# Performance work log

Hardware: AMD Instinct MI355X
Metric: run time of the kernel (lower is better)

Reference implementation:

```python
import jax, jax.numpy as jnp
import numpy as np
import math

N_HEAD = 8
N_EMBD = 1024
HEAD_DIM = N_EMBD // N_HEAD // 2  # 64
LAYER_IDX = 4
LAMBDA_INIT = 0.8 - 0.6 * math.exp(-0.3 * LAYER_IDX)
RMS_EPS = float(jnp.finfo(jnp.float32).eps)  # torch RMSNorm eps=None default
LN_EPS = 1e-5


def rmsnorm(x):
    return x * jax.lax.rsqrt(jnp.mean(x * x, axis=-1, keepdims=True) + RMS_EPS)


def layernorm(x):
    mu = jnp.mean(x, axis=-1, keepdims=True)
    var = jnp.mean(jnp.square(x - mu), axis=-1, keepdims=True)
    return (x - mu) * jax.lax.rsqrt(var + LN_EPS)


def rope_tables(T, dim, dtype):
    inv_freq = 1.0 / (10000.0 ** (np.arange(0, dim, 2, dtype=np.float32) / dim))
    t = np.arange(T, dtype=np.float32)
    freqs = np.outer(t, inv_freq)  # [T, dim/2]
    return jnp.asarray(np.cos(freqs), dtype), jnp.asarray(np.sin(freqs), dtype)


def apply_rotary(x, cos, sin):
    # x: [B, T, H, D]; cos/sin: [T, D/2]
    d = x.shape[-1] // 2
    x1, x2 = x[..., :d], x[..., d:]
    c = cos[None, :, None, :]
    s = sin[None, :, None, :]
    return jnp.concatenate([x1 * c + x2 * s, -x1 * s + x2 * c], axis=-1)


def setup_inputs() -> dict:
    key = jax.random.key(0)
    ks = jax.random.split(key, 9)
    B, T, C = 4, 2048, N_EMBD
    scale = 1.0 / math.sqrt(C)
    return {
        "x": jax.random.normal(ks[0], (B, T, C), jnp.float32),
        "Wq": jax.random.normal(ks[1], (C, C), jnp.float32) * scale,
        "Wk": jax.random.normal(ks[2], (C, C), jnp.float32) * scale,
        "Wv": jax.random.normal(ks[3], (C, C), jnp.float32) * scale,
        "Wproj": jax.random.normal(ks[4], (C, C), jnp.float32) * scale,
        "lq1": jax.random.normal(ks[5], (HEAD_DIM,), jnp.float32) * 0.1,
        "lk1": jax.random.normal(ks[6], (HEAD_DIM,), jnp.float32) * 0.1,
        "lq2": jax.random.normal(ks[7], (HEAD_DIM,), jnp.float32) * 0.1,
        "lk2": jax.random.normal(ks[8], (HEAD_DIM,), jnp.float32) * 0.1,
    }


def reference(x, Wq, Wk, Wv, Wproj, lq1, lk1, lq2, lk2):
    B, T, C = x.shape
    H, hd = N_HEAD, HEAD_DIM
    q = (x @ Wq.T).reshape(B, T, 2 * H, hd)
    k = (x @ Wk.T).reshape(B, T, 2 * H, hd)
    v = (x @ Wv.T).reshape(B, T, H, 2 * hd)

    cos, sin = rope_tables(T, hd, x.dtype)
    q = apply_rotary(rmsnorm(q), cos, sin)
    k = apply_rotary(rmsnorm(k), cos, sin)

    q = jnp.transpose(q, (0, 2, 1, 3)) * (1.0 / math.sqrt(hd))  # [B, 2H, T, hd]
    k = jnp.transpose(k, (0, 2, 1, 3))
    v = jnp.transpose(v, (0, 2, 1, 3))  # [B, H, T, 2hd]

    scores = jnp.einsum('bhqd,bhkd->bhqk', q, k)  # [B, 2H, T, T]
    causal = jnp.tril(jnp.ones((T, T), bool))
    scores = jnp.where(causal[None, None], scores, -jnp.inf)
    attn = jax.nn.softmax(scores.astype(jnp.float32), axis=-1).astype(scores.dtype)

    attn = attn.reshape(B, H, 2, T, T)
    lam1 = jnp.exp(jnp.sum(lq1 * lk1))
    lam2 = jnp.exp(jnp.sum(lq2 * lk2))
    lam = lam1 - lam2 + LAMBDA_INIT
    attn = attn[:, :, 0] - lam * attn[:, :, 1]  # [B, H, T, T]

    out = jnp.einsum('bhqk,bhkd->bhqd', attn, v)  # [B, H, T, 2hd]
    out = layernorm(out) * (1.0 - LAMBDA_INIT)
    out = jnp.transpose(out, (0, 2, 1, 3)).reshape(B, T, C)
    return out @ Wproj.T
```

## Files before the change

kernel.cpp:

```cpp
#include <hip/hip_runtime.h>
#include <hip/hip_bf16.h>
#include <math.h>


typedef __bf16 bf16_t;
typedef __bf16 bf16x8 __attribute__((ext_vector_type(8)));
typedef __bf16 bf16x4 __attribute__((ext_vector_type(4)));
typedef float  f32x4  __attribute__((ext_vector_type(4)));

#define T_SEQ 2048
#define C_EMB 1024
static constexpr float LAMBDA_INIT = 0.6192834728526787f;
static constexpr float ONE_MINUS_LI = 0.3807165271473213f;
static constexpr float RMS_EPS = 1.1920928955078125e-07f;
static constexpr float LN_EPS = 1e-5f;
static constexpr float M_FIX = 9.0f;

__device__ __forceinline__ f32x4 mfma16(bf16x8 a, bf16x8 b, f32x4 c) {
  return __builtin_amdgcn_mfma_f32_16x16x32_bf16(a, b, c, 0, 0, 0);
}
__device__ __forceinline__ float declamp(float v, float lim) {
  return fminf(fmaxf(v, -lim), lim);
}
__device__ __forceinline__ void ldsload16(const bf16_t* g, bf16_t* l) {
  __builtin_amdgcn_global_load_lds(
      (const __attribute__((address_space(1))) void*)g,
      (__attribute__((address_space(3))) void*)l, 16, 0, 0);
}


__global__ __launch_bounds__(256) void cvt_all(
    const float* __restrict__ x,  const float* __restrict__ Wq,
    const float* __restrict__ Wk, const float* __restrict__ Wv,
    const float* __restrict__ Wp,
    bf16_t* __restrict__ xb,  bf16_t* __restrict__ wqb, bf16_t* __restrict__ wkb,
    bf16_t* __restrict__ wvb, bf16_t* __restrict__ wpb)
{
  size_t i4 = ((size_t)blockIdx.x * 256 + threadIdx.x) * 4;
  const float* s; bf16_t* d; size_t off;
  if      (i4 <  8388608) { s = x;  d = xb;  off = i4; }
  else if (i4 <  9437184) { s = Wq; d = wqb; off = i4 - 8388608; }
  else if (i4 < 10485760) { s = Wk; d = wkb; off = i4 - 9437184; }
  else if (i4 < 11534336) { s = Wv; d = wvb; off = i4 - 10485760; }
  else                    { s = Wp; d = wpb; off = i4 - 11534336; }
  f32x4 v = *(const f32x4*)(s + off);
  bf16x4 bv;
#pragma unroll
  for (int j = 0; j < 4; ++j) bv[j] = (bf16_t)v[j];
  *(bf16x4*)(d + off) = bv;
}

__device__ __forceinline__ void gemm_core(
    const bf16_t* __restrict__ A, const bf16_t* __restrict__ W,
    bf16_t* As, bf16_t* Bs, f32x4 acc[4][4], int m0, int n0)
{
  const int tid = threadIdx.x;
  const int lane = tid & 63, w = tid >> 6;
  const int wm = w >> 1, wn = w & 1;
  const int l15 = lane & 15, quad = lane >> 4;
  for (int k0 = 0; k0 < C_EMB; k0 += 32) {
#pragma unroll
    for (int i = 0; i < 2; ++i) {
      int c = tid + i * 256;
      int r = c >> 2, c8 = (c & 3) * 8;
      *(bf16x8*)&As[r * 40 + c8] = *(const bf16x8*)&A[(size_t)(m0 + r) * C_EMB + k0 + c8];
      *(bf16x8*)&Bs[r * 40 + c8] = *(const bf16x8*)&W[(size_t)(n0 + r) * C_EMB + k0 + c8];
    }
    __syncthreads();
    bf16x8 af[4], bfr[4];
#pragma unroll
    for (int i = 0; i < 4; ++i)
      af[i] = *(const bf16x8*)&As[(wm * 64 + i * 16 + l15) * 40 + quad * 8];
#pragma unroll
    for (int j = 0; j < 4; ++j)
      bfr[j] = *(const bf16x8*)&Bs[(wn * 64 + j * 16 + l15) * 40 + quad * 8];
#pragma unroll
    for (int i = 0; i < 4; ++i)
#pragma unroll
      for (int j = 0; j < 4; ++j) acc[i][j] = mfma16(af[i], bfr[j], acc[i][j]);
    __syncthreads();
  }
}

__global__ __launch_bounds__(256) void gemm_qkv(
    const bf16_t* __restrict__ A,
    const bf16_t* __restrict__ Wqb, const bf16_t* __restrict__ Wkb, const bf16_t* __restrict__ Wvb,
    bf16_t* __restrict__ qo, bf16_t* __restrict__ ko, bf16_t* __restrict__ vt)
{
  const int z = blockIdx.z;
  const bf16_t* W = (z == 0) ? Wqb : ((z == 1) ? Wkb : Wvb);
  const int n0 = blockIdx.x * 128, m0 = blockIdx.y * 128;
  __shared__ bf16_t As[128 * 40];
  __shared__ bf16_t Bs[128 * 40];
  const int lane = threadIdx.x & 63, w = threadIdx.x >> 6;
  const int wm = w >> 1, wn = w & 1;
  const int l15 = lane & 15, quad = lane >> 4;
  const f32x4 fz = {0.f, 0.f, 0.f, 0.f};
  f32x4 acc[4][4];
#pragma unroll
  for (int i = 0; i < 4; ++i)
#pragma unroll
    for (int j = 0; j < 4; ++j) acc[i][j] = fz;
  gemm_core(A, W, As, Bs, acc, m0, n0);

  if (z < 2) {
    bf16_t* C = z ? ko : qo;
#pragma unroll
    for (int i = 0; i < 4; ++i)
#pragma unroll
      for (int j = 0; j < 4; ++j)
#pragma unroll
        for (int r = 0; r < 4; ++r) {
          int row = m0 + wm * 64 + i * 16 + quad * 4 + r;
          int col = n0 + wn * 64 + j * 16 + l15;
          C[(size_t)row * C_EMB + col] = (bf16_t)declamp(acc[i][j][r], 1e4f);
        }
  } else {
#pragma unroll
    for (int i = 0; i < 4; ++i)
#pragma unroll
      for (int j = 0; j < 4; ++j) {
        int row = m0 + wm * 64 + i * 16 + quad * 4;
        int col = n0 + wn * 64 + j * 16 + l15;
        bf16x4 pv;
#pragma unroll
        for (int r = 0; r < 4; ++r) pv[r] = (bf16_t)declamp(acc[i][j][r], 1e4f);
        size_t idx = (size_t)(row >> 11) * 2097152 + (size_t)col * 2048 + (row & 2047);
        *(bf16x4*)&vt[idx] = pv;
      }
  }
}

__global__ __launch_bounds__(256) void gemm_proj(
    const bf16_t* __restrict__ A, const bf16_t* __restrict__ Wpb, float* __restrict__ C)
{
  const int n0 = blockIdx.x * 128, m0 = blockIdx.y * 128;
  __shared__ bf16_t As[128 * 40];
  __shared__ bf16_t Bs[128 * 40];
  const int lane = threadIdx.x & 63, w = threadIdx.x >> 6;
  const int wm = w >> 1, wn = w & 1;
  const int l15 = lane & 15, quad = lane >> 4;
  const f32x4 fz = {0.f, 0.f, 0.f, 0.f};
  f32x4 acc[4][4];
#pragma unroll
  for (int i = 0; i < 4; ++i)
#pragma unroll
    for (int j = 0; j < 4; ++j) acc[i][j] = fz;
  gemm_core(A, Wpb, As, Bs, acc, m0, n0);
#pragma unroll
  for (int i = 0; i < 4; ++i)
#pragma unroll
    for (int j = 0; j < 4; ++j)
#pragma unroll
      for (int r = 0; r < 4; ++r) {
        int row = m0 + wm * 64 + i * 16 + quad * 4 + r;
        int col = n0 + wn * 64 + j * 16 + l15;
        C[(size_t)row * C_EMB + col] = declamp(acc[i][j][r], 1e4f);
      }
}

__global__ __launch_bounds__(256) void rope_rms2(bf16_t* __restrict__ q, bf16_t* __restrict__ k)
{
  bf16_t* arr = blockIdx.y ? k : q;
  const float scale = blockIdx.y ? 1.0f : 0.125f;
  const int tid = threadIdx.x;
  const int g = blockIdx.x * 16 + (tid >> 4);
  const int l16 = tid & 15;
  const int t = (g >> 4) & (T_SEQ - 1);
  bf16_t* p = arr + (size_t)g * 64 + l16 * 4;

  bf16x4 xv = *(const bf16x4*)p;
  float x[4];
#pragma unroll
  for (int j = 0; j < 4; ++j) x[j] = (float)xv[j];
  float ss = x[0]*x[0] + x[1]*x[1] + x[2]*x[2] + x[3]*x[3];
#pragma unroll
  for (int mm = 1; mm <= 8; mm <<= 1) ss += __shfl_xor(ss, mm);
  const float rn = rsqrtf(fmaxf(ss, 0.f) * (1.0f / 64.0f) + RMS_EPS);
  float nrm[4], prt[4];
#pragma unroll
  for (int j = 0; j < 4; ++j) nrm[j] = x[j] * rn;
#pragma unroll
  for (int j = 0; j < 4; ++j) prt[j] = __shfl_xor(nrm[j], 8);

  const int ib = (l16 & 7) * 4;
  const float sgn = (l16 < 8) ? 1.f : -1.f;
  bf16x4 ov;
#pragma unroll
  for (int j = 0; j < 4; ++j) {
    int i = ib + j;
    float invf = expf(-(float)i * 0.28782313662425575f);
    float ang = (float)t * invf;
    float c = cosf(ang), s = sinf(ang);
    ov[j] = (bf16_t)((nrm[j] * c + sgn * prt[j] * s) * scale);
  }
  *(bf16x4*)p = ov;
}

__device__ __forceinline__ void attn_step_fm(
    const bf16_t* __restrict__ ks, bf16_t* __restrict__ pw, const bf16_t* __restrict__ vts,
    const bf16x8* qf, float* rsum, f32x4* o,
    bool diag, int k0, int q0, int w, int l15, int quad)
{
  const int xs = l15 & 7;
  f32x4 sc[4];
#pragma unroll
  for (int nt = 0; nt < 4; ++nt) {
    f32x4 a = {0.f, 0.f, 0.f, 0.f};
#pragma unroll
    for (int s = 0; s < 2; ++s) {
      bf16x8 b = *(const bf16x8*)&ks[(nt * 16 + l15) * 64 + ((((s << 2) + quad) ^ xs) << 3)];
      a = mfma16(qf[s], b, a);
    }
#pragma unroll
    for (int r = 0; r < 4; ++r) a[r] = declamp(a[r], 30.f);
    sc[nt] = a;
  }
  if (diag) {
#pragma unroll
    for (int nt = 0; nt < 4; ++nt)
#pragma unroll
      for (int r = 0; r < 4; ++r) {
        int col = k0 + nt * 16 + l15;
        int row = q0 + w * 16 + quad * 4 + r;
        if (col > row) sc[nt][r] = -1e30f;
      }
  }
#pragma unroll
  for (int nt = 0; nt < 4; ++nt)
#pragma unroll
    for (int r = 0; r < 4; ++r) {
      float pv = __expf(sc[nt][r] - M_FIX);
      rsum[r] += pv;
      int row = quad * 4 + r;
      int col = nt * 16 + l15;
      pw[row * 64 + ((((col >> 3) ^ (row & 7)) << 3) | (col & 7))] = (bf16_t)pv;
    }
  __builtin_amdgcn_s_setprio(1);
#pragma unroll
  for (int s = 0; s < 2; ++s) {
    bf16x8 pa = *(const bf16x8*)&pw[l15 * 64 + ((((s << 2) + quad) ^ xs) << 3)];
#pragma unroll
    for (int nt2 = 0; nt2 < 8; ++nt2) {
      bf16x8 vb = *(const bf16x8*)&vts[(nt2 * 16 + l15) * 64 + ((((s << 2) + quad) ^ xs) << 3)];
      o[nt2] = mfma16(pa, vb, o[nt2]);
    }
  }
  __builtin_amdgcn_s_setprio(0);
}

__global__ __launch_bounds__(256) void diff_attn2(
    const bf16_t* __restrict__ qp, const bf16_t* __restrict__ kp, const bf16_t* __restrict__ vtp,
    const float* __restrict__ lq1, const float* __restrict__ lk1,
    const float* __restrict__ lq2, const float* __restrict__ lk2,
    bf16_t* __restrict__ outp)
{
  const int bh = blockIdx.x;
  const int bx = 31 - blockIdx.y;
  const int b = bh >> 3, h = bh & 7;
  const int q0 = bx * 64;
  const int tid = threadIdx.x;
  const int lane = tid & 63, w = tid >> 6;
  const int l15 = lane & 15, quad = lane >> 4;
  const size_t bT = (size_t)b * T_SEQ;
  const bf16_t* vth = vtp + (size_t)b * 2097152 + (size_t)(h * 128) * 2048;

  __shared__ bf16_t k1s[2][64 * 64];
  __shared__ bf16_t k2s[2][64 * 64];
  __shared__ bf16_t vts[2][128 * 64];
  __shared__ bf16_t ps[4][16 * 64];

  float e1 = lq1[lane] * lk1[lane];
  float e2 = lq2[lane] * lk2[lane];
#pragma unroll
  for (int mm = 1; mm <= 32; mm <<= 1) { e1 += __shfl_xor(e1, mm); e2 += __shfl_xor(e2, mm); }
  const float lam = expf(declamp(e1, 30.f)) - expf(declamp(e2, 30.f)) + LAMBDA_INIT;

  const int sh1 = 2 * h, sh2 = 2 * h + 1;

  const int lrow = lane >> 3;
  const int lchk = (lane & 7) ^ lrow;
  const bf16_t* k1g = kp + (bT + (size_t)(w * 16 + lrow)) * 1024 + sh1 * 64 + (lchk << 3);
  const bf16_t* k2g = kp + (bT + (size_t)(w * 16 + lrow)) * 1024 + sh2 * 64 + (lchk << 3);
  const bf16_t* vg  = vth + (size_t)(w * 32 + lrow) * 2048 + (lchk << 3);

  ldsload16(k1g,         &k1s[0][w * 1024]);
  ldsload16(k1g + 8192,  &k1s[0][w * 1024 + 512]);
  ldsload16(k2g,         &k2s[0][w * 1024]);
  ldsload16(k2g + 8192,  &k2s[0][w * 1024 + 512]);
  ldsload16(vg,          &vts[0][w * 2048]);
  ldsload16(vg + 16384,  &vts[0][w * 2048 + 512]);
  ldsload16(vg + 32768,  &vts[0][w * 2048 + 1024]);
  ldsload16(vg + 49152,  &vts[0][w * 2048 + 1536]);

  const int tq = q0 + w * 16 + l15;
  const bf16_t* qrow = qp + (bT + tq) * 1024;
  bf16x8 q1f[2], q2f[2];
#pragma unroll
  for (int s = 0; s < 2; ++s) {
    q1f[s] = *(const bf16x8*)&qrow[sh1 * 64 + s * 32 + quad * 8];
    q2f[s] = *(const bf16x8*)&qrow[sh2 * 64 + s * 32 + quad * 8];
  }

  const f32x4 fz = {0.f, 0.f, 0.f, 0.f};
  f32x4 o1[8], o2[8];
  float rs1[4] = {0, 0, 0, 0}, rs2[4] = {0, 0, 0, 0};
#pragma unroll
  for (int i = 0; i < 8; ++i) { o1[i] = fz; o2[i] = fz; }

  for (int kt = 0; kt <= bx; ++kt) {
    const int cur = kt & 1;
    __syncthreads();
    if (kt < bx) {
      const int nb = cur ^ 1;
      const bf16_t* s1 = k1g + (size_t)(kt + 1) * 65536;
      const bf16_t* s2 = k2g + (size_t)(kt + 1) * 65536;
      const bf16_t* sv = vg + (size_t)(kt + 1) * 64;
      ldsload16(s1,         &k1s[nb][w * 1024]);
      ldsload16(s1 + 8192,  &k1s[nb][w * 1024 + 512]);
      ldsload16(s2,         &k2s[nb][w * 1024]);
      ldsload16(s2 + 8192,  &k2s[nb][w * 1024 + 512]);
      ldsload16(sv,         &vts[nb][w * 2048]);
      ldsload16(sv + 16384, &vts[nb][w * 2048 + 512]);
      ldsload16(sv + 32768, &vts[nb][w * 2048 + 1024]);
      ldsload16(sv + 49152, &vts[nb][w * 2048 + 1536]);
    }
    const int k0 = kt * 64;
    const bool diag = (kt == bx);
    attn_step_fm(&k1s[cur][0], ps[w], &vts[cur][0], q1f, rs1, o1, diag, k0, q0, w, l15, quad);
    attn_step_fm(&k2s[cur][0], ps[w], &vts[cur][0], q2f, rs2, o2, diag, k0, q0, w, l15, quad);
  }

#pragma unroll
  for (int mm = 1; mm <= 8; mm <<= 1)
#pragma unroll
    for (int r = 0; r < 4; ++r) { rs1[r] += __shfl_xor(rs1[r], mm); rs2[r] += __shfl_xor(rs2[r], mm); }
  float i1[4], i2[4];
#pragma unroll
  for (int r = 0; r < 4; ++r) { i1[r] = 1.f / rs1[r]; i2[r] = 1.f / rs2[r]; }
  f32x4 od[8];
  float sum[4] = {0, 0, 0, 0}, sq[4] = {0, 0, 0, 0};
#pragma unroll
  for (int nt2 = 0; nt2 < 8; ++nt2)
#pragma unroll
    for (int r = 0; r < 4; ++r) {
      float v = declamp(o1[nt2][r] * i1[r] - lam * o2[nt2][r] * i2[r], 1e4f);
      od[nt2][r] = v;
      sum[r] += v;
      sq[r] += v * v;
    }
#pragma unroll
  for (int mm = 1; mm <= 8; mm <<= 1)
#pragma unroll
    for (int r = 0; r < 4; ++r) { sum[r] += __shfl_xor(sum[r], mm); sq[r] += __shfl_xor(sq[r], mm); }
  float mu[4], scl[4];
#pragma unroll
  for (int r = 0; r < 4; ++r) {
    mu[r] = sum[r] * (1.0f / 128.0f);
    float var = sq[r] * (1.0f / 128.0f) - mu[r] * mu[r];
    scl[r] = rsqrtf(fmaxf(var, 0.f) + LN_EPS) * ONE_MINUS_LI;
  }
#pragma unroll
  for (int nt2 = 0; nt2 < 8; ++nt2)
#pragma unroll
    for (int r = 0; r < 4; ++r) {
      int trow = q0 + w * 16 + quad * 4 + r;
      outp[(bT + trow) * 1024 + h * 128 + nt2 * 16 + l15] =
          (bf16_t)((od[nt2][r] - mu[r]) * scl[r]);
    }
}


__device__ __forceinline__ void attn_step(
    const bf16_t* __restrict__ ks, bf16_t* __restrict__ pw, const bf16_t* __restrict__ vts,
    const bf16x8* qf, float* mR, float* lR, f32x4* o,
    bool diag, int k0, int q0, int w, int l15, int quad)
{
  f32x4 sc[4];
#pragma unroll
  for (int nt = 0; nt < 4; ++nt) {
    f32x4 a = {0.f, 0.f, 0.f, 0.f};
#pragma unroll
    for (int s = 0; s < 2; ++s) {
      bf16x8 b = *(const bf16x8*)&ks[(nt * 16 + l15) * 72 + s * 32 + quad * 8];
      a = mfma16(qf[s], b, a);
    }
#pragma unroll
    for (int r = 0; r < 4; ++r) a[r] = declamp(a[r], 1e4f);
    sc[nt] = a;
  }
  if (diag) {
#pragma unroll
    for (int nt = 0; nt < 4; ++nt)
#pragma unroll
      for (int r = 0; r < 4; ++r) {
        int col = k0 + nt * 16 + l15;
        int row = q0 + w * 16 + quad * 4 + r;
        if (col > row) sc[nt][r] = -1e30f;
      }
  }
  float mx[4];
#pragma unroll
  for (int r = 0; r < 4; ++r)
    mx[r] = fmaxf(fmaxf(sc[0][r], sc[1][r]), fmaxf(sc[2][r], sc[3][r]));
#pragma unroll
  for (int mm = 1; mm <= 8; mm <<= 1)
#pragma unroll
    for (int r = 0; r < 4; ++r) mx[r] = fmaxf(mx[r], __shfl_xor(mx[r], mm));

  float mnew[4], alpha[4], rs[4];
#pragma unroll
  for (int r = 0; r < 4; ++r) {
    mnew[r] = fmaxf(mR[r], mx[r]);
    alpha[r] = __expf(mR[r] - mnew[r]);
    rs[r] = 0.f;
  }
#pragma unroll
  for (int nt = 0; nt < 4; ++nt)
#pragma unroll
    for (int r = 0; r < 4; ++r) {
      float pv = __expf(sc[nt][r] - mnew[r]);
      rs[r] += pv;
      pw[(quad * 4 + r) * 72 + nt * 16 + l15] = (bf16_t)pv;
    }
#pragma unroll
  for (int mm = 1; mm <= 8; mm <<= 1)
#pragma unroll
    for (int r = 0; r < 4; ++r) rs[r] += __shfl_xor(rs[r], mm);
#pragma unroll
  for (int r = 0; r < 4; ++r) {
    lR[r] = lR[r] * alpha[r] + rs[r];
    mR[r] = mnew[r];
  }
#pragma unroll
  for (int nt2 = 0; nt2 < 8; ++nt2)
#pragma unroll
    for (int r = 0; r < 4; ++r) o[nt2][r] *= alpha[r];
#pragma unroll
  for (int s = 0; s < 2; ++s) {
    bf16x8 pa = *(const bf16x8*)&pw[l15 * 72 + s * 32 + quad * 8];
#pragma unroll
    for (int nt2 = 0; nt2 < 8; ++nt2) {
      bf16x8 vb = *(const bf16x8*)&vts[(nt2 * 16 + l15) * 72 + s * 32 + quad * 8];
      o[nt2] = mfma16(pa, vb, o[nt2]);
    }
  }
}

template<bool A_F32, bool OUT_F32>
__global__ __launch_bounds__(256) void gemm_bt(
    const void* __restrict__ Ap,
    const float* __restrict__ W0, const float* __restrict__ W1, const float* __restrict__ W2,
    void* __restrict__ Cp0, void* __restrict__ Cp1, void* __restrict__ Cp2)
{
  const float* W = (blockIdx.z == 0) ? W0 : ((blockIdx.z == 1) ? W1 : W2);
  void*       Cv = (blockIdx.z == 0) ? Cp0 : ((blockIdx.z == 1) ? Cp1 : Cp2);
  const int K = C_EMB, N = C_EMB;
  const int n0 = blockIdx.x * 128, m0 = blockIdx.y * 128;
  __shared__ bf16_t As[128 * 40];
  __shared__ bf16_t Bs[128 * 40];
  const int tid = threadIdx.x;
  const int lane = tid & 63, w = tid >> 6;
  const int wm = w >> 1, wn = w & 1;
  const int l15 = lane & 15, quad = lane >> 4;
  const f32x4 fz = {0.f, 0.f, 0.f, 0.f};
  f32x4 acc[4][4];
#pragma unroll
  for (int i = 0; i < 4; ++i)
#pragma unroll
    for (int j = 0; j < 4; ++j) acc[i][j] = fz;

  for (int k0 = 0; k0 < K; k0 += 32) {
    if constexpr (A_F32) {
      const float* Af = (const float*)Ap;
#pragma unroll
      for (int i = 0; i < 4; ++i) {
        int c = tid + i * 256;
        int r = c >> 3, c4 = (c & 7) * 4;
        f32x4 v = *(const f32x4*)&Af[(size_t)(m0 + r) * K + k0 + c4];
        bf16x4 bv;
#pragma unroll
        for (int j = 0; j < 4; ++j) bv[j] = (bf16_t)v[j];
        *(bf16x4*)&As[r * 40 + c4] = bv;
      }
    } else {
      const bf16_t* Ab = (const bf16_t*)Ap;
#pragma unroll
      for (int i = 0; i < 2; ++i) {
        int c = tid + i * 256;
        int r = c >> 2, c8 = (c & 3) * 8;
        *(bf16x8*)&As[r * 40 + c8] = *(const bf16x8*)&Ab[(size_t)(m0 + r) * K + k0 + c8];
      }
    }
#pragma unroll
    for (int i = 0; i < 4; ++i) {
      int c = tid + i * 256;
      int r = c >> 3, c4 = (c & 7) * 4;
      f32x4 v = *(const f32x4*)&W[(size_t)(n0 + r) * K + k0 + c4];
      bf16x4 bv;
#pragma unroll
      for (int j = 0; j < 4; ++j) bv[j] = (bf16_t)v[j];
      *(bf16x4*)&Bs[r * 40 + c4] = bv;
    }
    __syncthreads();
    bf16x8 af[4], bfr[4];
#pragma unroll
    for (int i = 0; i < 4; ++i)
      af[i] = *(const bf16x8*)&As[(wm * 64 + i * 16 + l15) * 40 + quad * 8];
#pragma unroll
    for (int j = 0; j < 4; ++j)
      bfr[j] = *(const bf16x8*)&Bs[(wn * 64 + j * 16 + l15) * 40 + quad * 8];
#pragma unroll
    for (int i = 0; i < 4; ++i)
#pragma unroll
      for (int j = 0; j < 4; ++j) acc[i][j] = mfma16(af[i], bfr[j], acc[i][j]);
    __syncthreads();
  }
#pragma unroll
  for (int i = 0; i < 4; ++i)
#pragma unroll
    for (int j = 0; j < 4; ++j)
#pragma unroll
      for (int r = 0; r < 4; ++r) {
        int row = m0 + wm * 64 + i * 16 + quad * 4 + r;
        int col = n0 + wn * 64 + j * 16 + l15;
        float v = declamp(acc[i][j][r], 1e4f);
        if constexpr (OUT_F32) ((float*)Cv)[(size_t)row * N + col] = v;
        else                   ((bf16_t*)Cv)[(size_t)row * N + col] = (bf16_t)v;
      }
}

__global__ __launch_bounds__(256) void rope_rms(bf16_t* __restrict__ arr, int is_q)
{
  const int tid = threadIdx.x;
  const int g = blockIdx.x * 16 + (tid >> 4);
  const int l16 = tid & 15;
  const int t = (g >> 4) & (T_SEQ - 1);
  bf16_t* p = arr + (size_t)g * 64 + l16 * 4;
  bf16x4 xv = *(const bf16x4*)p;
  float x[4];
#pragma unroll
  for (int j = 0; j < 4; ++j) x[j] = (float)xv[j];
  float ss = x[0]*x[0] + x[1]*x[1] + x[2]*x[2] + x[3]*x[3];
#pragma unroll
  for (int mm = 1; mm <= 8; mm <<= 1) ss += __shfl_xor(ss, mm);
  const float rn = rsqrtf(fmaxf(ss, 0.f) * (1.0f / 64.0f) + RMS_EPS);
  float nrm[4], prt[4];
#pragma unroll
  for (int j = 0; j < 4; ++j) nrm[j] = x[j] * rn;
#pragma unroll
  for (int j = 0; j < 4; ++j) prt[j] = __shfl_xor(nrm[j], 8);
  const int ib = (l16 & 7) * 4;
  const float sgn = (l16 < 8) ? 1.f : -1.f;
  const float scale = is_q ? 0.125f : 1.0f;
  bf16x4 ov;
#pragma unroll
  for (int j = 0; j < 4; ++j) {
    int i = ib + j;
    float invf = expf(-(float)i * 0.28782313662425575f);
    float ang = (float)t * invf;
    float c = cosf(ang), s = sinf(ang);
    ov[j] = (bf16_t)((nrm[j] * c + sgn * prt[j] * s) * scale);
  }
  *(bf16x4*)p = ov;
}

__global__ __launch_bounds__(256) void diff_attn(
    const bf16_t* qp, const bf16_t* __restrict__ kp, const bf16_t* __restrict__ vp,
    const float* __restrict__ lq1, const float* __restrict__ lk1,
    const float* __restrict__ lq2, const float* __restrict__ lk2,
    bf16_t* outp)
{
  const int bx = blockIdx.x;
  const int h = blockIdx.y;
  const int q0 = bx * 64;
  const int tid = threadIdx.x;
  const int lane = tid & 63, w = tid >> 6;
  const int l15 = lane & 15, quad = lane >> 4;

  __shared__ bf16_t k1s[64 * 72];
  __shared__ bf16_t k2s[64 * 72];
  __shared__ bf16_t vts[128 * 72];
  __shared__ bf16_t ps[4][16 * 72];

  float e1 = lq1[lane] * lk1[lane];
  float e2 = lq2[lane] * lk2[lane];
#pragma unroll
  for (int mm = 1; mm <= 32; mm <<= 1) { e1 += __shfl_xor(e1, mm); e2 += __shfl_xor(e2, mm); }
  const float lam = expf(declamp(e1, 30.f)) - expf(declamp(e2, 30.f)) + LAMBDA_INIT;

  const int sh1 = 2 * h, sh2 = 2 * h + 1;
  const int tq = q0 + w * 16 + l15;
  const bf16_t* qrow = qp + (size_t)tq * 1024;
  bf16x8 q1f[2], q2f[2];
#pragma unroll
  for (int s = 0; s < 2; ++s) {
    q1f[s] = *(const bf16x8*)&qrow[sh1 * 64 + s * 32 + quad * 8];
    q2f[s] = *(const bf16x8*)&qrow[sh2 * 64 + s * 32 + quad * 8];
  }
  const f32x4 fz = {0.f, 0.f, 0.f, 0.f};
  f32x4 o1[8], o2[8];
  float m1[4], l1[4], m2[4], l2[4];
#pragma unroll
  for (int i = 0; i < 8; ++i) { o1[i] = fz; o2[i] = fz; }
#pragma unroll
  for (int r = 0; r < 4; ++r) { m1[r] = -1e30f; m2[r] = -1e30f; l1[r] = 0.f; l2[r] = 0.f; }

  for (int kt = 0; kt <= bx; ++kt) {
    const int k0 = kt * 64;
    __syncthreads();
#pragma unroll
    for (int i = 0; i < 2; ++i) {
      int c = tid + i * 256;
      int r = c >> 3, c8 = (c & 7) * 8;
      const bf16_t* krow = kp + (size_t)(k0 + r) * 1024;
      *(bf16x8*)&k1s[r * 72 + c8] = *(const bf16x8*)&krow[sh1 * 64 + c8];
      *(bf16x8*)&k2s[r * 72 + c8] = *(const bf16x8*)&krow[sh2 * 64 + c8];
    }
#pragma unroll
    for (int i = 0; i < 4; ++i) {
      int c = tid + i * 256;
      int r = c >> 4, d8 = (c & 15) * 8;
      bf16x8 vv = *(const bf16x8*)&vp[(size_t)(k0 + r) * 1024 + h * 128 + d8];
#pragma unroll
      for (int jj = 0; jj < 8; ++jj) vts[(d8 + jj) * 72 + r] = vv[jj];
    }
    __syncthreads();
    const bool diag = (kt == bx);
    attn_step(k1s, ps[w], vts, q1f, m1, l1, o1, diag, k0, q0, w, l15, quad);
    attn_step(k2s, ps[w], vts, q2f, m2, l2, o2, diag, k0, q0, w, l15, quad);
  }
  float i1[4], i2[4];
#pragma unroll
  for (int r = 0; r < 4; ++r) { i1[r] = 1.f / l1[r]; i2[r] = 1.f / l2[r]; }
  f32x4 od[8];
  float sum[4] = {0, 0, 0, 0}, sq[4] = {0, 0, 0, 0};
#pragma unroll
  for (int nt2 = 0; nt2 < 8; ++nt2)
#pragma unroll
    for (int r = 0; r < 4; ++r) {
      float v = declamp(o1[nt2][r] * i1[r] - lam * o2[nt2][r] * i2[r], 1e4f);
      od[nt2][r] = v;
      sum[r] += v;
      sq[r] += v * v;
    }
#pragma unroll
  for (int mm = 1; mm <= 8; mm <<= 1)
#pragma unroll
    for (int r = 0; r < 4; ++r) { sum[r] += __shfl_xor(sum[r], mm); sq[r] += __shfl_xor(sq[r], mm); }
  float mu[4], scl[4];
#pragma unroll
  for (int r = 0; r < 4; ++r) {
    mu[r] = sum[r] * (1.0f / 128.0f);
    float var = sq[r] * (1.0f / 128.0f) - mu[r] * mu[r];
    scl[r] = rsqrtf(fmaxf(var, 0.f) + LN_EPS) * ONE_MINUS_LI;
  }
#pragma unroll
  for (int nt2 = 0; nt2 < 8; ++nt2)
#pragma unroll
    for (int r = 0; r < 4; ++r) {
      int trow = q0 + w * 16 + quad * 4 + r;
      outp[(size_t)trow * 1024 + h * 128 + nt2 * 16 + l15] =
          (bf16_t)((od[nt2][r] - mu[r]) * scl[r]);
    }
}

extern "C" void kernel_launch(void* const* d_in, const int* in_sizes, int n_in,
                              void* d_out, int out_size, void* d_ws, size_t ws_size,
                              hipStream_t stream) {
  const float* x     = (const float*)d_in[0];
  const float* Wq    = (const float*)d_in[1];
  const float* Wk    = (const float*)d_in[2];
  const float* Wv    = (const float*)d_in[3];
  const float* Wproj = (const float*)d_in[4];
  const float* lq1   = (const float*)d_in[5];
  const float* lk1   = (const float*)d_in[6];
  const float* lq2   = (const float*)d_in[7];
  const float* lk2   = (const float*)d_in[8];
  float* O = (float*)d_out;
  const size_t R = (size_t)T_SEQ * C_EMB;

  if (ws_size >= (size_t)40 * 1024 * 1024) {
    bf16_t* wsb = (bf16_t*)d_ws;
    bf16_t* xb  = wsb;
    bf16_t* wqb = wsb + 8388608;
    bf16_t* wkb = wqb + 1048576;
    bf16_t* wvb = wkb + 1048576;
    bf16_t* wpb = wvb + 1048576;
    bf16_t* vt  = wpb + 1048576;
    bf16_t* qo  = (bf16_t*)d_out;
    bf16_t* ko  = qo + 8388608;
    bf16_t* a   = xb;

    cvt_all<<<12288, 256, 0, stream>>>(x, Wq, Wk, Wv, Wproj, xb, wqb, wkb, wvb, wpb);
    gemm_qkv<<<dim3(8, 64, 3), 256, 0, stream>>>(xb, wqb, wkb, wvb, qo, ko, vt);
    rope_rms2<<<dim3(8192, 2), 256, 0, stream>>>(qo, ko);
    diff_attn2<<<dim3(32, 32), 256, 0, stream>>>(qo, ko, vt, lq1, lk1, lq2, lk2, a);
    gemm_proj<<<dim3(8, 64), 256, 0, stream>>>(a, wpb, O);
  } else {
    char* Ob = (char*)d_out;
    char* Xb = (char*)d_in[0];
    const size_t MB4 = (size_t)1 << 22;
    bf16_t* qb[4] = { (bf16_t*)(Ob + 2*MB4), (bf16_t*)(Ob + 5*MB4),
                      (bf16_t*)(Xb + 0*MB4), (bf16_t*)(Xb + 3*MB4) };
    bf16_t* kb[4] = { (bf16_t*)(Ob + 3*MB4), (bf16_t*)(Ob + 6*MB4),
                      (bf16_t*)(Xb + 1*MB4), (bf16_t*)(Xb + 4*MB4) };
    bf16_t* vb[4] = { (bf16_t*)(Ob + 4*MB4), (bf16_t*)(Ob + 7*MB4),
                      (bf16_t*)(Xb + 2*MB4), (bf16_t*)(Xb + 5*MB4) };
    for (int b = 0; b < 4; ++b) {
      const float* xbp = x + (size_t)b * R;
      gemm_bt<true, false><<<dim3(8, 16, 3), 256, 0, stream>>>(
          xbp, Wq, Wk, Wv, qb[b], kb[b], vb[b]);
      rope_rms<<<2048, 256, 0, stream>>>(qb[b], 1);
      rope_rms<<<2048, 256, 0, stream>>>(kb[b], 0);
      diff_attn<<<dim3(32, 8), 256, 0, stream>>>(qb[b], kb[b], vb[b],
                                                 lq1, lk1, lq2, lk2, qb[b]);
      gemm_bt<false, true><<<dim3(8, 16, 1), 256, 0, stream>>>(
          qb[b], Wproj, Wproj, Wproj, O + (size_t)b * R, nullptr, nullptr);
    }
  }
}
```

Before: 336.1 us.

## Double-buffer GEMM LDS tiles with async loads, swizzle, and XCD tile remap

The shared GEMM core now uses a double-buffered, XOR-swizzled LDS layout filled by direct global-to-LDS loads, so the next K-slice is prefetched while MFMAs run on the current one. A barrier is dropped per iteration and MFMA issue priority is raised. Block indices are remapped so tiles are grouped in a new order, likely to improve L2 locality across XCDs. The rotary embedding switches to fast __expf/__sincosf intrinsics, which trades a little accuracy at large angles.

```diff
diff --git a/kernel.cpp b/kernel.cpp
--- a/kernel.cpp
+++ b/kernel.cpp
@@ -52,34 +52,60 @@
 
 __device__ __forceinline__ void gemm_core(
     const bf16_t* __restrict__ A, const bf16_t* __restrict__ W,
-    bf16_t* As, bf16_t* Bs, f32x4 acc[4][4], int m0, int n0)
+    bf16_t (*As)[4096], bf16_t (*Bs)[4096], f32x4 acc[4][4], int m0, int n0)
 {
   const int tid = threadIdx.x;
   const int lane = tid & 63, w = tid >> 6;
   const int wm = w >> 1, wn = w & 1;
   const int l15 = lane & 15, quad = lane >> 4;
-  for (int k0 = 0; k0 < C_EMB; k0 += 32) {
-#pragma unroll
-    for (int i = 0; i < 2; ++i) {
-      int c = tid + i * 256;
-      int r = c >> 2, c8 = (c & 3) * 8;
-      *(bf16x8*)&As[r * 40 + c8] = *(const bf16x8*)&A[(size_t)(m0 + r) * C_EMB + k0 + c8];
-      *(bf16x8*)&Bs[r * 40 + c8] = *(const bf16x8*)&W[(size_t)(n0 + r) * C_EMB + k0 + c8];
-    }
+
+  const int srow = lane >> 2;
+  const int schk = (lane & 3) ^ ((lane >> 3) & 3);
+  const bf16_t* Ag = A + (size_t)(m0 + w * 32 + srow) * C_EMB + schk * 8;
+  const bf16_t* Wg = W + (size_t)(n0 + w * 32 + srow) * C_EMB + schk * 8;
+
+  ldsload16(Ag,              &As[0][w * 1024]);
+  ldsload16(Ag + 16 * C_EMB, &As[0][w * 1024 + 512]);
+  ldsload16(Wg,              &Bs[0][w * 1024]);
+  ldsload16(Wg + 16 * C_EMB, &Bs[0][w * 1024 + 512]);
+
+  for (int ks = 0; ks < 32; ++ks) {
+    const int cur = ks & 1;
     __syncthreads();
+    if (ks < 31) {
+      const int nb = cur ^ 1;
+      const bf16_t* a2 = Ag + (ks + 1) * 32;
+      const bf16_t* w2 = Wg + (ks + 1) * 32;
+      ldsload16(a2,              &As[nb][w * 1024]);
+      ldsload16(a2 + 16 * C_EMB, &As[nb][w * 1024 + 512]);
+      ldsload16(w2,              &Bs[nb][w * 1024]);
+      ldsload16(w2 + 16 * C_EMB, &Bs[nb][w * 1024 + 512]);
+    }
     bf16x8 af[4], bfr[4];
 #pragma unroll
+    for (int i = 0; i < 4; ++i) {
+      int ra = wm * 64 + i * 16 + l15;
+      int ca = quad ^ ((ra >> 1) & 3);
+      af[i] = *(const bf16x8*)&As[cur][ra * 32 + ca * 8];
+    }
+#pragma unroll
+    for (int j = 0; j < 4; ++j) {
+      int rb = wn * 64 + j * 16 + l15;
+      int cb = quad ^ ((rb >> 1) & 3);
+      bfr[j] = *(const bf16x8*)&Bs[cur][rb * 32 + cb * 8];
+    }
+    __builtin_amdgcn_s_setprio(1);
+#pragma unroll
     for (int i = 0; i < 4; ++i)
-      af[i] = *(const bf16x8*)&As[(wm * 64 + i * 16 + l15) * 40 + quad * 8];
-#pragma unroll
-    for (int j = 0; j < 4; ++j)
-      bfr[j] = *(const bf16x8*)&Bs[(wn * 64 + j * 16 + l15) * 40 + quad * 8];
-#pragma unroll
-    for (int i = 0; i < 4; ++i)
 #pragma unroll
       for (int j = 0; j < 4; ++j) acc[i][j] = mfma16(af[i], bfr[j], acc[i][j]);
-    __syncthreads();
-  }
+    __builtin_amdgcn_s_setprio(0);
+  }
+}
+
+__device__ __forceinline__ void xcd_tiles(int& m0, int& n0) {
+  m0 = (blockIdx.x * 8 + (blockIdx.y >> 3)) * 128;
+  n0 = (blockIdx.y & 7) * 128;
 }
 
 __global__ __launch_bounds__(256) void gemm_qkv(
@@ -89,9 +115,9 @@
 {
   const int z = blockIdx.z;
   const bf16_t* W = (z == 0) ? Wqb : ((z == 1) ? Wkb : Wvb);
-  const int n0 = blockIdx.x * 128, m0 = blockIdx.y * 128;
-  __shared__ bf16_t As[128 * 40];
-  __shared__ bf16_t Bs[128 * 40];
+  int m0, n0; xcd_tiles(m0, n0);
+  __shared__ bf16_t As[2][4096];
+  __shared__ bf16_t Bs[2][4096];
   const int lane = threadIdx.x & 63, w = threadIdx.x >> 6;
   const int wm = w >> 1, wn = w & 1;
   const int l15 = lane & 15, quad = lane >> 4;
@@ -134,9 +160,9 @@
 __global__ __launch_bounds__(256) void gemm_proj(
     const bf16_t* __restrict__ A, const bf16_t* __restrict__ Wpb, float* __restrict__ C)
 {
-  const int n0 = blockIdx.x * 128, m0 = blockIdx.y * 128;
-  __shared__ bf16_t As[128 * 40];
-  __shared__ bf16_t Bs[128 * 40];
+  int m0, n0; xcd_tiles(m0, n0);
+  __shared__ bf16_t As[2][4096];
+  __shared__ bf16_t Bs[2][4096];
   const int lane = threadIdx.x & 63, w = threadIdx.x >> 6;
   const int wm = w >> 1, wn = w & 1;
   const int l15 = lane & 15, quad = lane >> 4;
@@ -189,9 +215,10 @@
 #pragma unroll
   for (int j = 0; j < 4; ++j) {
     int i = ib + j;
-    float invf = expf(-(float)i * 0.28782313662425575f);
+    float invf = __expf(-(float)i * 0.28782313662425575f);
     float ang = (float)t * invf;
-    float c = cosf(ang), s = sinf(ang);
+    float c, s;
+    __sincosf(ang, &s, &c);
     ov[j] = (bf16_t)((nrm[j] * c + sgn * prt[j] * s) * scale);
   }
   *(bf16x4*)p = ov;
@@ -557,9 +584,10 @@
 #pragma unroll
   for (int j = 0; j < 4; ++j) {
     int i = ib + j;
-    float invf = expf(-(float)i * 0.28782313662425575f);
+    float invf = __expf(-(float)i * 0.28782313662425575f);
     float ang = (float)t * invf;
-    float c = cosf(ang), s = sinf(ang);
+    float c, s;
+    __sincosf(ang, &s, &c);
     ov[j] = (bf16_t)((nrm[j] * c + sgn * prt[j] * s) * scale);
   }
   *(bf16x4*)p = ov;
```

Result: faster. 304.0 us (-9.5%).
